# Kernel optimization log

Measured on AMD Instinct MI355X. Metric: run time of the kernel, lower is better.

The kernel has to match this reference:

```python
import jax, jax.numpy as jnp
import numpy as np

N_NODES = 50000


def gcn_conv(x, src, dst, W, b, n_nodes):
    """PyG-style GCNConv: x' = D^-1/2 (A + I) D^-1/2 (x W) + b.
    src/dst already include self-loops."""
    h = x @ W  # [N, C_out]
    # symmetric normalization from degree (with self-loops, unit edge weight)
    deg = jax.ops.segment_sum(jnp.ones_like(dst, dtype=h.dtype), dst,
                              num_segments=n_nodes)  # [N]
    dinv = jnp.where(deg > 0, jax.lax.rsqrt(deg), 0.0)
    norm = dinv[src] * dinv[dst]  # [E]
    msg = h[src] * norm[:, None]  # gather + scale, [E, C_out]
    out = jax.ops.segment_sum(msg, dst, num_segments=n_nodes)  # scatter-add
    return out + b


def setup_inputs() -> dict:
    key = jax.random.key(0)
    k1, k2, k3, k4, k5, k6 = jax.random.split(key, 6)
    in_c, hid_c, out_c = 128, 64, 64
    x = jax.random.normal(k1, (N_NODES, in_c), dtype=jnp.float32)
    edge_index = jax.random.randint(k2, (2, 800000), 0, N_NODES, dtype=jnp.int64)
    # Glorot-ish init for weights, zeros for bias (as PyG default)
    W1 = jax.random.normal(k3, (in_c, hid_c), dtype=jnp.float32) / np.sqrt(in_c)
    b1 = jnp.zeros((hid_c,), dtype=jnp.float32)
    W2 = jax.random.normal(k4, (hid_c, out_c), dtype=jnp.float32) / np.sqrt(hid_c)
    b2 = jnp.zeros((out_c,), dtype=jnp.float32)
    return {"x": x, "edge_index": edge_index, "W1": W1, "b1": b1,
            "W2": W2, "b2": b2}


def reference(x, edge_index, W1, b1, W2, b2):
    n = x.shape[0]
    loops = jnp.arange(n, dtype=edge_index.dtype)
    src = jnp.concatenate([edge_index[0], loops])  # add self-loops
    dst = jnp.concatenate([edge_index[1], loops])
    h = gcn_conv(x, src, dst, W1, b1, n)
    h = jax.nn.relu(h)
    return gcn_conv(h, src, dst, W2, b2, n)
```

## Files before the change

kernel.cpp:

```cpp
#include <hip/hip_runtime.h>
#include <hip/hip_fp16.h>


#define C_HID 64
#define NCHUNK 512
#define ES3 1280
#define ES4 768

static inline size_t alignup(size_t x) { return (x + 255) & ~(size_t)255; }

typedef __attribute__((address_space(3))) unsigned int lds_uint;
typedef __attribute__((address_space(1))) const unsigned int glob_uint;

__device__ __forceinline__ int blockScanIncl256(int v, int* wsum) {
    const int lane = threadIdx.x & 63, wav = threadIdx.x >> 6;
    int s = v;
#pragma unroll
    for (int off = 1; off < 64; off <<= 1) {
        int t = __shfl_up(s, off);
        if (lane >= off) s += t;
    }
    if (lane == 63) wsum[wav] = s;
    __syncthreads();
    if (wav == 0 && lane < 4) {
        int ws = wsum[lane];
#pragma unroll
        for (int off = 1; off < 4; off <<= 1) {
            int t = __shfl_up(ws, off);
            if (lane >= off) ws += t;
        }
        wsum[lane] = ws;
    }
    __syncthreads();
    return (wav ? wsum[wav - 1] : 0) + s;
}

template <int K>
__global__ __launch_bounds__(256) void gemm1_hist_kernel(
    const float* __restrict__ X, const float* __restrict__ W,
    const int* __restrict__ dst, __half* __restrict__ outh,
    int* __restrict__ S, int n, int E, int ePer, int nb) {
    constexpr int KP = K + 4;
    __shared__ float Xs[64 * KP];
    __shared__ float Ws[K * 64];
    __shared__ int h[1024];
    const int t = threadIdx.x;
    const int lane = t & 63;
    const int wav = t >> 6;

    if ((int)blockIdx.x < NCHUNK) {
        for (int i = t; i < nb; i += 256) h[i] = 0;
        __syncthreads();
        int beg = blockIdx.x * ePer, end = min(E, beg + ePer);
        for (int e = beg + t; e < end; e += 256)
            atomicAdd(&h[dst[e] >> 6], 1);
        __syncthreads();
        for (int b = t; b < nb; b += 256)
            S[(size_t)b * NCHUNK + blockIdx.x] = h[b];
        return;
    }

    const int row0 = ((int)blockIdx.x - NCHUNK) * 64;
    {
        const char* gb = (const char*)W;
        char* lb = (char*)Ws;
        for (int off = wav * 1024; off < K * 64 * 4; off += 4096)
            __builtin_amdgcn_global_load_lds((glob_uint*)(gb + off + lane * 16),
                                             (lds_uint*)(lb + off), 16, 0, 0);
    }
    if (row0 + 64 <= n) {
        const float4* g4 = (const float4*)(X + (size_t)row0 * K);
        for (int i = t; i < 64 * (K / 4); i += 256) {
            float4 v = g4[i];
            int r = i / (K / 4), k0 = (i % (K / 4)) * 4;
            *(float4*)&Xs[r * KP + k0] = v;
        }
    } else {
        for (int i = t; i < 64 * K; i += 256) {
            int r = i / K, k = i % K;
            Xs[r * KP + k] = (row0 + r < n) ? X[(size_t)(row0 + r) * K + k] : 0.0f;
        }
    }
    __syncthreads();

    const int tx = t & 15;
    const int ty = t >> 4;
    float acc[4][4] = {{0.f}};
#pragma unroll 2
    for (int k0 = 0; k0 < K; k0 += 4) {
        float4 a0 = *(const float4*)&Xs[(4 * ty + 0) * KP + k0];
        float4 a1 = *(const float4*)&Xs[(4 * ty + 1) * KP + k0];
        float4 a2 = *(const float4*)&Xs[(4 * ty + 2) * KP + k0];
        float4 a3 = *(const float4*)&Xs[(4 * ty + 3) * KP + k0];
        float4 b0 = *(const float4*)&Ws[(k0 + 0) * 64 + 4 * tx];
        float4 b1 = *(const float4*)&Ws[(k0 + 1) * 64 + 4 * tx];
        float4 b2 = *(const float4*)&Ws[(k0 + 2) * 64 + 4 * tx];
        float4 b3 = *(const float4*)&Ws[(k0 + 3) * 64 + 4 * tx];
        const float* ap[4] = {(const float*)&a0, (const float*)&a1,
                              (const float*)&a2, (const float*)&a3};
        const float* bp[4] = {(const float*)&b0, (const float*)&b1,
                              (const float*)&b2, (const float*)&b3};
#pragma unroll
        for (int r = 0; r < 4; ++r)
#pragma unroll
            for (int kk = 0; kk < 4; ++kk) {
                float av = ap[r][kk];
#pragma unroll
                for (int c = 0; c < 4; ++c)
                    acc[r][c] = fmaf(av, bp[kk][c], acc[r][c]);
            }
    }
#pragma unroll
    for (int r = 0; r < 4; ++r) {
        int row = row0 + 4 * ty + r;
        if (row < n) {
            __half2 p01 = __floats2half2_rn(acc[r][0], acc[r][1]);
            __half2 p23 = __floats2half2_rn(acc[r][2], acc[r][3]);
            float2 st;
            ((__half2*)&st)[0] = p01;
            ((__half2*)&st)[1] = p23;
            *(float2*)&outh[(size_t)row * 64 + 4 * tx] = st;
        }
    }
}

__global__ __launch_bounds__(256) void scan_rows_kernel(
    int* __restrict__ S, int* __restrict__ T) {
    __shared__ int wsum[4];
    const int b = blockIdx.x, t = threadIdx.x;
    int4 v = make_int4(0, 0, 0, 0);
    if (t < NCHUNK / 4) v = ((const int4*)(S + (size_t)b * NCHUNK))[t];
    int p1 = v.x + v.y, p2 = p1 + v.z, p3 = p2 + v.w;
    int incl = blockScanIncl256(p3, wsum);
    int excl = incl - p3;
    if (t < NCHUNK / 4) {
        int4 o;
        o.x = excl; o.y = excl + v.x; o.z = excl + p1; o.w = excl + p2;
        ((int4*)(S + (size_t)b * NCHUNK))[t] = o;
    }
    if (t == 0) T[b] = wsum[3];
}

__global__ __launch_bounds__(256) void scatter_kernel(
    const int* __restrict__ src, const int* __restrict__ dst, int E, int ePer,
    const int* __restrict__ S, const int* __restrict__ T,
    unsigned* __restrict__ ebuf, int nb) {
    __shared__ int tmp[1024];
    __shared__ int arr[1024];
    __shared__ int wsum[4];
    const int b = blockIdx.x, t = threadIdx.x;
    {
        int a0 = (4 * t + 0 < nb) ? T[4 * t + 0] : 0;
        int a1 = (4 * t + 1 < nb) ? T[4 * t + 1] : 0;
        int a2 = (4 * t + 2 < nb) ? T[4 * t + 2] : 0;
        int a3 = (4 * t + 3 < nb) ? T[4 * t + 3] : 0;
        int p1 = a0 + a1, p2 = p1 + a2, p3 = p2 + a3;
        int incl = blockScanIncl256(p3, wsum);
        int excl = incl - p3;
        tmp[4 * t + 0] = excl;
        tmp[4 * t + 1] = excl + a0;
        tmp[4 * t + 2] = excl + p1;
        tmp[4 * t + 3] = excl + p2;
    }
    __syncthreads();
    for (int i = t; i < nb; i += 256)
        arr[i] = S[(size_t)i * NCHUNK + b] + tmp[i];
    __syncthreads();
    int beg = b * ePer, end = min(E, beg + ePer);
    for (int e = beg + t; e < end; e += 256) {
        int d = dst[e];
        int s = src[e];
        int pos = atomicAdd(&arr[d >> 6], 1);
        ebuf[pos] = ((unsigned)s << 6) | (unsigned)(d & 63);
    }
}

__global__ __launch_bounds__(256) void build_kernel(
    const unsigned* __restrict__ ebuf, const int* __restrict__ T,
    int* __restrict__ row_ptr, float* __restrict__ dinv,
    int* __restrict__ esrc, __half* __restrict__ g1, int n, int nb) {
    __shared__ int tmp[1024];
    __shared__ int cnt[64];
    __shared__ int cur[64];
    __shared__ float dvs[64];
    __shared__ int wsum[4];
    const int b = blockIdx.x, t = threadIdx.x;
    {
        int a0 = (4 * t + 0 < nb) ? T[4 * t + 0] : 0;
        int a1 = (4 * t + 1 < nb) ? T[4 * t + 1] : 0;
        int a2 = (4 * t + 2 < nb) ? T[4 * t + 2] : 0;
        int a3 = (4 * t + 3 < nb) ? T[4 * t + 3] : 0;
        int p1 = a0 + a1, p2 = p1 + a2, p3 = p2 + a3;
        int incl = blockScanIncl256(p3, wsum);
        int excl = incl - p3;
        tmp[4 * t + 0] = excl + a0;
        tmp[4 * t + 1] = excl + p1;
        tmp[4 * t + 2] = excl + p2;
        tmp[4 * t + 3] = excl + p3;
    }
    if (t < 64) cnt[t] = 0;
    __syncthreads();
    const int ebeg = b ? tmp[b - 1] : 0;
    const int eend = tmp[b];

    for (int e = ebeg + t; e < eend; e += 256)
        atomicAdd(&cnt[ebuf[e] & 63], 1);
    __syncthreads();
    if (t < 64) {
        int deg = cnt[t];
        int s = deg;
#pragma unroll
        for (int off = 1; off < 64; off <<= 1) {
            int x = __shfl_up(s, off);
            if (t >= off) s += x;
        }
        cur[t] = ebeg + s - deg;
        float dv = rsqrtf(1.0f + (float)deg);
        dvs[t] = dv;
        int v = (b << 6) + t;
        if (v < n) {
            row_ptr[v + 1] = ebeg + s;
            dinv[v] = dv;
            if (v == 0) row_ptr[0] = 0;
        }
    }
    __syncthreads();
    for (int e = ebeg + t; e < eend; e += 256) {
        unsigned p = ebuf[e];
        int pos = atomicAdd(&cur[p & 63], 1);
        esrc[pos] = (int)(p >> 6);
    }
    {
        const int row = t >> 2, q = t & 3;
        const int v = (b << 6) + row;
        if (v < n) {
            float dv = dvs[row];
            float4* gp = (float4*)(g1 + (size_t)v * 64 + q * 16);
            float4 r0 = gp[0], r1 = gp[1];
            __half2* h0 = (__half2*)&r0;
            __half2* h1 = (__half2*)&r1;
#pragma unroll
            for (int i2 = 0; i2 < 4; ++i2) {
                float2 f0 = __half22float2(h0[i2]);
                float2 f1 = __half22float2(h1[i2]);
                h0[i2] = __floats2half2_rn(f0.x * dv, f0.y * dv);
                h1[i2] = __floats2half2_rn(f1.x * dv, f1.y * dv);
            }
            gp[0] = r0;
            gp[1] = r1;
        }
    }
}

template <bool LDSE>
__device__ __forceinline__ void agg1_body(
    const float4* __restrict__ hs4, const int* es, const int* __restrict__ esg,
    int beg0, int beg, int end, int c, float acc[16]) {
    int j = beg;
    for (; j + 4 <= end; j += 4) {
        int s0, s1, s2, s3;
        if (LDSE) {
            s0 = es[j]; s1 = es[j + 1]; s2 = es[j + 2]; s3 = es[j + 3];
        } else {
            s0 = esg[beg0 + j]; s1 = esg[beg0 + j + 1];
            s2 = esg[beg0 + j + 2]; s3 = esg[beg0 + j + 3];
        }
        size_t rb0 = (size_t)s0 * 8 + 2 * c, rb1 = (size_t)s1 * 8 + 2 * c;
        size_t rb2 = (size_t)s2 * 8 + 2 * c, rb3 = (size_t)s3 * 8 + 2 * c;
        float4 a0 = hs4[rb0], a1 = hs4[rb0 + 1];
        float4 b0 = hs4[rb1], b1v = hs4[rb1 + 1];
        float4 c0 = hs4[rb2], c1 = hs4[rb2 + 1];
        float4 e0 = hs4[rb3], e1 = hs4[rb3 + 1];
        const __half2 *pa0 = (const __half2*)&a0, *pa1 = (const __half2*)&a1;
        const __half2 *pb0 = (const __half2*)&b0, *pb1 = (const __half2*)&b1v;
        const __half2 *pc0 = (const __half2*)&c0, *pc1 = (const __half2*)&c1;
        const __half2 *pe0 = (const __half2*)&e0, *pe1 = (const __half2*)&e1;
#pragma unroll
        for (int q = 0; q < 4; ++q) {
            float2 f;
            f = __half22float2(pa0[q]); acc[2 * q] += f.x; acc[2 * q + 1] += f.y;
            f = __half22float2(pa1[q]); acc[8 + 2 * q] += f.x; acc[9 + 2 * q] += f.y;
            f = __half22float2(pb0[q]); acc[2 * q] += f.x; acc[2 * q + 1] += f.y;
            f = __half22float2(pb1[q]); acc[8 + 2 * q] += f.x; acc[9 + 2 * q] += f.y;
            f = __half22float2(pc0[q]); acc[2 * q] += f.x; acc[2 * q + 1] += f.y;
            f = __half22float2(pc1[q]); acc[8 + 2 * q] += f.x; acc[9 + 2 * q] += f.y;
            f = __half22float2(pe0[q]); acc[2 * q] += f.x; acc[2 * q + 1] += f.y;
            f = __half22float2(pe1[q]); acc[8 + 2 * q] += f.x; acc[9 + 2 * q] += f.y;
        }
    }
    for (; j < end; ++j) {
        int s0 = LDSE ? es[j] : esg[beg0 + j];
        size_t rb0 = (size_t)s0 * 8 + 2 * c;
        float4 a0 = hs4[rb0], a1 = hs4[rb0 + 1];
        const __half2 *pa0 = (const __half2*)&a0, *pa1 = (const __half2*)&a1;
#pragma unroll
        for (int q = 0; q < 4; ++q) {
            float2 f;
            f = __half22float2(pa0[q]); acc[2 * q] += f.x; acc[2 * q + 1] += f.y;
            f = __half22float2(pa1[q]); acc[8 + 2 * q] += f.x; acc[9 + 2 * q] += f.y;
        }
    }
}

__global__ __launch_bounds__(256) void agg1_gemm2_kernel(
    const __half* __restrict__ g1, const int* __restrict__ row_ptr,
    const int* __restrict__ esrc, const float* __restrict__ dinv,
    const float* __restrict__ b1, const float* __restrict__ W2,
    __half* __restrict__ g2, int n) {
    __shared__ float Bt[64][68];
    __shared__ float Ws2[64 * 64];
    __shared__ int es[ES3];
    const int t = threadIdx.x, lane = t & 63, wav = t >> 6;
    const int row0 = blockIdx.x * 64;

    const int beg0 = row_ptr[row0];
    const int end0 = row_ptr[min(row0 + 64, n)];
    const int tot = end0 - beg0;
    const bool uselds = (tot <= ES3);
    if (uselds)
        for (int i = t; i < tot; i += 256) es[i] = esrc[beg0 + i];
    __syncthreads();

    {
        const char* gb = (const char*)W2;
        char* lb = (char*)Ws2;
        for (int off = wav * 1024; off < 64 * 64 * 4; off += 4096)
            __builtin_amdgcn_global_load_lds((glob_uint*)(gb + off + lane * 16),
                                             (lds_uint*)(lb + off), 16, 0, 0);
    }

    const int g = t >> 2;
    const int c = t & 3;
    const int v = row0 + g;
    const float4* __restrict__ hs4 = (const float4*)g1;

    if (v < n) {
        float acc[16];
        {
            size_t rb = (size_t)v * 8 + 2 * c;
            float4 r0 = hs4[rb], r1 = hs4[rb + 1];
            const __half2* h0 = (const __half2*)&r0;
            const __half2* h1 = (const __half2*)&r1;
#pragma unroll
            for (int q = 0; q < 4; ++q) {
                float2 f0 = __half22float2(h0[q]);
                float2 f1 = __half22float2(h1[q]);
                acc[2 * q] = f0.x;     acc[2 * q + 1] = f0.y;
                acc[8 + 2 * q] = f1.x; acc[9 + 2 * q] = f1.y;
            }
        }
        const int beg = row_ptr[v] - beg0;
        const int end = row_ptr[v + 1] - beg0;
        if (uselds) agg1_body<true>(hs4, es, esrc, beg0, beg, end, c, acc);
        else        agg1_body<false>(hs4, es, esrc, beg0, beg, end, c, acc);
        const float dv0 = dinv[v];
        const float* bb = b1 + c * 16;
#pragma unroll
        for (int u = 0; u < 4; ++u) {
            float4 w;
            w.x = fmaxf(fmaf(acc[4 * u + 0], dv0, bb[4 * u + 0]), 0.f);
            w.y = fmaxf(fmaf(acc[4 * u + 1], dv0, bb[4 * u + 1]), 0.f);
            w.z = fmaxf(fmaf(acc[4 * u + 2], dv0, bb[4 * u + 2]), 0.f);
            w.w = fmaxf(fmaf(acc[4 * u + 3], dv0, bb[4 * u + 3]), 0.f);
            *(float4*)&Bt[g][c * 16 + 4 * u] = w;
        }
    } else {
#pragma unroll
        for (int u = 0; u < 4; ++u)
            *(float4*)&Bt[g][c * 16 + 4 * u] = make_float4(0.f, 0.f, 0.f, 0.f);
    }
    __syncthreads();

    const int tx = t & 15;
    const int ty = t >> 4;
    float a2[4][4] = {{0.f}};
#pragma unroll 2
    for (int k0 = 0; k0 < 64; k0 += 4) {
        float4 x0 = *(const float4*)&Bt[4 * ty + 0][k0];
        float4 x1 = *(const float4*)&Bt[4 * ty + 1][k0];
        float4 x2 = *(const float4*)&Bt[4 * ty + 2][k0];
        float4 x3 = *(const float4*)&Bt[4 * ty + 3][k0];
        float4 w0 = *(const float4*)&Ws2[(k0 + 0) * 64 + 4 * tx];
        float4 w1 = *(const float4*)&Ws2[(k0 + 1) * 64 + 4 * tx];
        float4 w2 = *(const float4*)&Ws2[(k0 + 2) * 64 + 4 * tx];
        float4 w3 = *(const float4*)&Ws2[(k0 + 3) * 64 + 4 * tx];
        const float* xp[4] = {(const float*)&x0, (const float*)&x1,
                              (const float*)&x2, (const float*)&x3};
        const float* wp[4] = {(const float*)&w0, (const float*)&w1,
                              (const float*)&w2, (const float*)&w3};
#pragma unroll
        for (int r = 0; r < 4; ++r)
#pragma unroll
            for (int kk = 0; kk < 4; ++kk) {
                float av = xp[r][kk];
#pragma unroll
                for (int cc = 0; cc < 4; ++cc)
                    a2[r][cc] = fmaf(av, wp[kk][cc], a2[r][cc]);
            }
    }
#pragma unroll
    for (int r = 0; r < 4; ++r) {
        int row = row0 + 4 * ty + r;
        if (row < n) {
            float dv = dinv[row];
            __half2 p01 = __floats2half2_rn(a2[r][0] * dv, a2[r][1] * dv);
            __half2 p23 = __floats2half2_rn(a2[r][2] * dv, a2[r][3] * dv);
            float2 st;
            ((__half2*)&st)[0] = p01;
            ((__half2*)&st)[1] = p23;
            *(float2*)&g2[(size_t)row * 64 + 4 * tx] = st;
        }
    }
}

template <bool LDSE>
__device__ __forceinline__ void agg2_body(
    const float4* __restrict__ hs4, const int* es, const int* __restrict__ esg,
    int beg0, int beg, int end, int c8, float acc[8]) {
    int j = beg;
    for (; j + 4 <= end; j += 4) {
        int s0, s1, s2, s3;
        if (LDSE) {
            s0 = es[j]; s1 = es[j + 1]; s2 = es[j + 2]; s3 = es[j + 3];
        } else {
            s0 = esg[beg0 + j]; s1 = esg[beg0 + j + 1];
            s2 = esg[beg0 + j + 2]; s3 = esg[beg0 + j + 3];
        }
        float4 r0 = hs4[(size_t)s0 * 8 + c8];
        float4 r1 = hs4[(size_t)s1 * 8 + c8];
        float4 r2 = hs4[(size_t)s2 * 8 + c8];
        float4 r3 = hs4[(size_t)s3 * 8 + c8];
        const __half2* h0 = (const __half2*)&r0;
        const __half2* h1 = (const __half2*)&r1;
        const __half2* h2 = (const __half2*)&r2;
        const __half2* h3 = (const __half2*)&r3;
#pragma unroll
        for (int q = 0; q < 4; ++q) {
            float2 f0 = __half22float2(h0[q]);
            float2 f1 = __half22float2(h1[q]);
            float2 f2 = __half22float2(h2[q]);
            float2 f3 = __half22float2(h3[q]);
            acc[2 * q]     += (f0.x + f1.x) + (f2.x + f3.x);
            acc[2 * q + 1] += (f0.y + f1.y) + (f2.y + f3.y);
        }
    }
    for (; j < end; ++j) {
        int s0 = LDSE ? es[j] : esg[beg0 + j];
        float4 r0 = hs4[(size_t)s0 * 8 + c8];
        const __half2* h0 = (const __half2*)&r0;
#pragma unroll
        for (int q = 0; q < 4; ++q) {
            float2 f0 = __half22float2(h0[q]);
            acc[2 * q] += f0.x;
            acc[2 * q + 1] += f0.y;
        }
    }
}

__global__ __launch_bounds__(256) void aggregate2_kernel(
    const __half* __restrict__ hs,
    const int* __restrict__ row_ptr,
    const int* __restrict__ esrc,
    const float* __restrict__ dinv,
    const float* __restrict__ bias,
    float* __restrict__ out, int n) {
    __shared__ int es[ES4];
    const int t = threadIdx.x;
    const int row0 = blockIdx.x * 32;
    const int beg0 = row_ptr[row0];
    const int end0 = row_ptr[min(row0 + 32, n)];
    const int tot = end0 - beg0;
    const bool uselds = (tot <= ES4);
    if (uselds)
        for (int i = t; i < tot; i += 256) es[i] = esrc[beg0 + i];
    __syncthreads();

    const int v = row0 + (t >> 3);
    if (v >= n) return;
    const int c8 = t & 7;
    const float4* __restrict__ hs4 = (const float4*)hs;

    float acc[8];
    {
        float4 raw = hs4[(size_t)v * 8 + c8];
        const __half2* hp = (const __half2*)&raw;
#pragma unroll
        for (int q = 0; q < 4; ++q) {
            float2 f = __half22float2(hp[q]);
            acc[2 * q] = f.x; acc[2 * q + 1] = f.y;
        }
    }

    const int beg = row_ptr[v] - beg0;
    const int end = row_ptr[v + 1] - beg0;
    if (uselds) agg2_body<true>(hs4, es, esrc, beg0, beg, end, c8, acc);
    else        agg2_body<false>(hs4, es, esrc, beg0, beg, end, c8, acc);

    float dv = dinv[v];
    float4 b0 = *(const float4*)(bias + c8 * 8);
    float4 b1v = *(const float4*)(bias + c8 * 8 + 4);
    float4 o0, o1;
    o0.x = fmaf(acc[0], dv, b0.x); o0.y = fmaf(acc[1], dv, b0.y);
    o0.z = fmaf(acc[2], dv, b0.z); o0.w = fmaf(acc[3], dv, b0.w);
    o1.x = fmaf(acc[4], dv, b1v.x); o1.y = fmaf(acc[5], dv, b1v.y);
    o1.z = fmaf(acc[6], dv, b1v.z); o1.w = fmaf(acc[7], dv, b1v.w);
    float4* op = (float4*)(out + (size_t)v * 64 + c8 * 8);
    op[0] = o0;
    op[1] = o1;
}

extern "C" void kernel_launch(void* const* d_in, const int* in_sizes, int n_in,
                              void* d_out, int out_size, void* d_ws, size_t ws_size,
                              hipStream_t stream) {
    const float* x  = (const float*)d_in[0];
    const int*   ei = (const int*)d_in[1];
    const float* W1 = (const float*)d_in[2];
    const float* b1 = (const float*)d_in[3];
    const float* W2 = (const float*)d_in[4];
    const float* b2 = (const float*)d_in[5];
    float* out = (float*)d_out;

    const int C_IN = 128;
    const int n = in_sizes[0] / C_IN;
    const int E = in_sizes[1] / 2;
    const int* src = ei;
    const int* dst = ei + E;

    const int nb = (n + 63) >> 6;
    const int ngb = (n + 63) / 64;
    const int ePer = (E + NCHUNK - 1) / NCHUNK;

    char* w = (char*)d_ws;
    float*    dinv    = (float*)w;    w += alignup((size_t)n * sizeof(float));
    __half*   g1      = (__half*)w;   w += alignup((size_t)n * C_HID * sizeof(__half));
    __half*   g2      = (__half*)w;   w += alignup((size_t)n * C_HID * sizeof(__half));
    int*      row_ptr = (int*)w;      w += alignup((size_t)(n + 1) * sizeof(int));
    int*      S       = (int*)w;      w += alignup((size_t)nb * NCHUNK * sizeof(int));
    int*      T       = (int*)w;      w += alignup((size_t)(nb + 1) * sizeof(int));
    unsigned* ebuf    = (unsigned*)w; w += alignup((size_t)E * sizeof(unsigned));
    int*      esrc    = (int*)w;

    gemm1_hist_kernel<128><<<NCHUNK + ngb, 256, 0, stream>>>(
        x, W1, dst, g1, S, n, E, ePer, nb);

    scan_rows_kernel<<<nb, 256, 0, stream>>>(S, T);
    scatter_kernel<<<NCHUNK, 256, 0, stream>>>(src, dst, E, ePer, S, T, ebuf, nb);
    build_kernel<<<nb, 256, 0, stream>>>(ebuf, T, row_ptr, dinv, esrc, g1, n, nb);

    agg1_gemm2_kernel<<<ngb, 256, 0, stream>>>(
        g1, row_ptr, esrc, dinv, b1, W2, g2, n);

    aggregate2_kernel<<<(n + 31) / 32, 256, 0, stream>>>(
        g2, row_ptr, esrc, dinv, b2, out, n);
}
```

Measured before the change: 163.9 us.

## Fuse scan, scatter, build and both aggregations into one persistent kernel with grid barriers

Replaces five separate launches (row scan, scatter, CSR build, agg1+gemm2, aggregate2) with one persistent 512-block kernel. The phases are separated by a software grid barrier built on an atomic counter, which the histogram kernel resets. The aim is to remove launch gaps and tail effects between the small dependent stages. Chunk count rises to 784 and layer-2 aggregation now uses 64-row tiles with four threads per row. The barrier depends on all 512 blocks being co-resident, which is risky, and blocks now loop serially over tiles.

```diff
diff --git a/kernel.cpp b/kernel.cpp
--- a/kernel.cpp
+++ b/kernel.cpp
@@ -3,14 +3,26 @@
 
 
 #define C_HID 64
-#define NCHUNK 512
+#define NCHUNK 784
+#define GMEGA 512
 #define ES3 1280
-#define ES4 768
 
 static inline size_t alignup(size_t x) { return (x + 255) & ~(size_t)255; }
 
 typedef __attribute__((address_space(3))) unsigned int lds_uint;
 typedef __attribute__((address_space(1))) const unsigned int glob_uint;
+
+__device__ __forceinline__ void gsync(unsigned* bar, unsigned target) {
+    __syncthreads();
+    if (threadIdx.x == 0) {
+        __threadfence();
+        atomicAdd(bar, 1u);
+        while (atomicAdd(bar, 0u) < target)
+            __builtin_amdgcn_s_sleep(8);
+        __threadfence();
+    }
+    __syncthreads();
+}
 
 __device__ __forceinline__ int blockScanIncl256(int v, int* wsum) {
     const int lane = threadIdx.x & 63, wav = threadIdx.x >> 6;
@@ -39,7 +51,8 @@
 __global__ __launch_bounds__(256) void gemm1_hist_kernel(
     const float* __restrict__ X, const float* __restrict__ W,
     const int* __restrict__ dst, __half* __restrict__ outh,
-    int* __restrict__ S, int n, int E, int ePer, int nb) {
+    int* __restrict__ S, unsigned* __restrict__ bar,
+    int n, int E, int ePer, int nb) {
     constexpr int KP = K + 4;
     __shared__ float Xs[64 * KP];
     __shared__ float Ws[K * 64];
@@ -49,6 +62,7 @@
     const int wav = t >> 6;
 
     if ((int)blockIdx.x < NCHUNK) {
+        if (blockIdx.x == 0 && t == 0) *bar = 0;
         for (int i = t; i < nb; i += 256) h[i] = 0;
         __syncthreads();
         int beg = blockIdx.x * ePer, end = min(E, beg + ePer);
@@ -124,134 +138,6 @@
     }
 }
 
-__global__ __launch_bounds__(256) void scan_rows_kernel(
-    int* __restrict__ S, int* __restrict__ T) {
-    __shared__ int wsum[4];
-    const int b = blockIdx.x, t = threadIdx.x;
-    int4 v = make_int4(0, 0, 0, 0);
-    if (t < NCHUNK / 4) v = ((const int4*)(S + (size_t)b * NCHUNK))[t];
-    int p1 = v.x + v.y, p2 = p1 + v.z, p3 = p2 + v.w;
-    int incl = blockScanIncl256(p3, wsum);
-    int excl = incl - p3;
-    if (t < NCHUNK / 4) {
-        int4 o;
-        o.x = excl; o.y = excl + v.x; o.z = excl + p1; o.w = excl + p2;
-        ((int4*)(S + (size_t)b * NCHUNK))[t] = o;
-    }
-    if (t == 0) T[b] = wsum[3];
-}
-
-__global__ __launch_bounds__(256) void scatter_kernel(
-    const int* __restrict__ src, const int* __restrict__ dst, int E, int ePer,
-    const int* __restrict__ S, const int* __restrict__ T,
-    unsigned* __restrict__ ebuf, int nb) {
-    __shared__ int tmp[1024];
-    __shared__ int arr[1024];
-    __shared__ int wsum[4];
-    const int b = blockIdx.x, t = threadIdx.x;
-    {
-        int a0 = (4 * t + 0 < nb) ? T[4 * t + 0] : 0;
-        int a1 = (4 * t + 1 < nb) ? T[4 * t + 1] : 0;
-        int a2 = (4 * t + 2 < nb) ? T[4 * t + 2] : 0;
-        int a3 = (4 * t + 3 < nb) ? T[4 * t + 3] : 0;
-        int p1 = a0 + a1, p2 = p1 + a2, p3 = p2 + a3;
-        int incl = blockScanIncl256(p3, wsum);
-        int excl = incl - p3;
-        tmp[4 * t + 0] = excl;
-        tmp[4 * t + 1] = excl + a0;
-        tmp[4 * t + 2] = excl + p1;
-        tmp[4 * t + 3] = excl + p2;
-    }
-    __syncthreads();
-    for (int i = t; i < nb; i += 256)
-        arr[i] = S[(size_t)i * NCHUNK + b] + tmp[i];
-    __syncthreads();
-    int beg = b * ePer, end = min(E, beg + ePer);
-    for (int e = beg + t; e < end; e += 256) {
-        int d = dst[e];
-        int s = src[e];
-        int pos = atomicAdd(&arr[d >> 6], 1);
-        ebuf[pos] = ((unsigned)s << 6) | (unsigned)(d & 63);
-    }
-}
-
-__global__ __launch_bounds__(256) void build_kernel(
-    const unsigned* __restrict__ ebuf, const int* __restrict__ T,
-    int* __restrict__ row_ptr, float* __restrict__ dinv,
-    int* __restrict__ esrc, __half* __restrict__ g1, int n, int nb) {
-    __shared__ int tmp[1024];
-    __shared__ int cnt[64];
-    __shared__ int cur[64];
-    __shared__ float dvs[64];
-    __shared__ int wsum[4];
-    const int b = blockIdx.x, t = threadIdx.x;
-    {
-        int a0 = (4 * t + 0 < nb) ? T[4 * t + 0] : 0;
-        int a1 = (4 * t + 1 < nb) ? T[4 * t + 1] : 0;
-        int a2 = (4 * t + 2 < nb) ? T[4 * t + 2] : 0;
-        int a3 = (4 * t + 3 < nb) ? T[4 * t + 3] : 0;
-        int p1 = a0 + a1, p2 = p1 + a2, p3 = p2 + a3;
-        int incl = blockScanIncl256(p3, wsum);
-        int excl = incl - p3;
-        tmp[4 * t + 0] = excl + a0;
-        tmp[4 * t + 1] = excl + p1;
-        tmp[4 * t + 2] = excl + p2;
-        tmp[4 * t + 3] = excl + p3;
-    }
-    if (t < 64) cnt[t] = 0;
-    __syncthreads();
-    const int ebeg = b ? tmp[b - 1] : 0;
-    const int eend = tmp[b];
-
-    for (int e = ebeg + t; e < eend; e += 256)
-        atomicAdd(&cnt[ebuf[e] & 63], 1);
-    __syncthreads();
-    if (t < 64) {
-        int deg = cnt[t];
-        int s = deg;
-#pragma unroll
-        for (int off = 1; off < 64; off <<= 1) {
-            int x = __shfl_up(s, off);
-            if (t >= off) s += x;
-        }
-        cur[t] = ebeg + s - deg;
-        float dv = rsqrtf(1.0f + (float)deg);
-        dvs[t] = dv;
-        int v = (b << 6) + t;
-        if (v < n) {
-            row_ptr[v + 1] = ebeg + s;
-            dinv[v] = dv;
-            if (v == 0) row_ptr[0] = 0;
-        }
-    }
-    __syncthreads();
-    for (int e = ebeg + t; e < eend; e += 256) {
-        unsigned p = ebuf[e];
-        int pos = atomicAdd(&cur[p & 63], 1);
-        esrc[pos] = (int)(p >> 6);
-    }
-    {
-        const int row = t >> 2, q = t & 3;
-        const int v = (b << 6) + row;
-        if (v < n) {
-            float dv = dvs[row];
-            float4* gp = (float4*)(g1 + (size_t)v * 64 + q * 16);
-            float4 r0 = gp[0], r1 = gp[1];
-            __half2* h0 = (__half2*)&r0;
-            __half2* h1 = (__half2*)&r1;
-#pragma unroll
-            for (int i2 = 0; i2 < 4; ++i2) {
-                float2 f0 = __half22float2(h0[i2]);
-                float2 f1 = __half22float2(h1[i2]);
-                h0[i2] = __floats2half2_rn(f0.x * dv, f0.y * dv);
-                h1[i2] = __floats2half2_rn(f1.x * dv, f1.y * dv);
-            }
-            gp[0] = r0;
-            gp[1] = r1;
-        }
-    }
-}
-
 template <bool LDSE>
 __device__ __forceinline__ void agg1_body(
     const float4* __restrict__ hs4, const int* es, const int* __restrict__ esg,
@@ -302,211 +188,288 @@
     }
 }
 
-__global__ __launch_bounds__(256) void agg1_gemm2_kernel(
-    const __half* __restrict__ g1, const int* __restrict__ row_ptr,
-    const int* __restrict__ esrc, const float* __restrict__ dinv,
-    const float* __restrict__ b1, const float* __restrict__ W2,
-    __half* __restrict__ g2, int n) {
-    __shared__ float Bt[64][68];
-    __shared__ float Ws2[64 * 64];
-    __shared__ int es[ES3];
+__global__ __launch_bounds__(256, 4) void mega_kernel(
+    const int* __restrict__ src, const int* __restrict__ dst, int E, int ePer,
+    int* __restrict__ S, int* __restrict__ T, unsigned* __restrict__ ebuf,
+    int* __restrict__ row_ptr, float* __restrict__ dinv, int* __restrict__ esrc,
+    __half* __restrict__ g1, const float* __restrict__ b1,
+    const float* __restrict__ W2, __half* __restrict__ g2,
+    const float* __restrict__ b2, float* __restrict__ out,
+    unsigned* __restrict__ bar, int n, int nb) {
+    __shared__ union SM {
+        struct { int tmp[1024]; int arr[1024]; } c;
+        struct { int tmp[1024]; int cnt[64]; int cur[64]; float dvs[64]; } d;
+        struct { float Bt[64][68]; float Ws2[64 * 64]; int es[ES3]; } e;
+        struct { int es[ES3]; } f;
+    } sm;
+    __shared__ int wsum[4];
     const int t = threadIdx.x, lane = t & 63, wav = t >> 6;
-    const int row0 = blockIdx.x * 64;
-
-    const int beg0 = row_ptr[row0];
-    const int end0 = row_ptr[min(row0 + 64, n)];
-    const int tot = end0 - beg0;
-    const bool uselds = (tot <= ES3);
-    if (uselds)
-        for (int i = t; i < tot; i += 256) es[i] = esrc[beg0 + i];
-    __syncthreads();
+    const int ngb = nb;
+    const int G = gridDim.x;
+
+    for (int b = blockIdx.x; b < nb; b += G) {
+        int4 v = make_int4(0, 0, 0, 0);
+        if (t < NCHUNK / 4) v = ((const int4*)(S + (size_t)b * NCHUNK))[t];
+        int p1 = v.x + v.y, p2 = p1 + v.z, p3 = p2 + v.w;
+        int incl = blockScanIncl256(p3, wsum);
+        int excl = incl - p3;
+        if (t < NCHUNK / 4) {
+            int4 o;
+            o.x = excl; o.y = excl + v.x; o.z = excl + p1; o.w = excl + p2;
+            ((int4*)(S + (size_t)b * NCHUNK))[t] = o;
+        }
+        if (t == 0) T[b] = wsum[3];
+        __syncthreads();
+    }
+    gsync(bar, 1u * G);
 
     {
         const char* gb = (const char*)W2;
-        char* lb = (char*)Ws2;
+        char* lb = (char*)sm.e.Ws2;
         for (int off = wav * 1024; off < 64 * 64 * 4; off += 4096)
             __builtin_amdgcn_global_load_lds((glob_uint*)(gb + off + lane * 16),
                                              (lds_uint*)(lb + off), 16, 0, 0);
     }
 
+    {
+        int a0 = (4 * t + 0 < nb) ? T[4 * t + 0] : 0;
+        int a1 = (4 * t + 1 < nb) ? T[4 * t + 1] : 0;
+        int a2 = (4 * t + 2 < nb) ? T[4 * t + 2] : 0;
+        int a3 = (4 * t + 3 < nb) ? T[4 * t + 3] : 0;
+        int p1 = a0 + a1, p2 = p1 + a2, p3 = p2 + a3;
+        int incl = blockScanIncl256(p3, wsum);
+        int excl = incl - p3;
+        sm.c.tmp[4 * t + 0] = excl;
+        sm.c.tmp[4 * t + 1] = excl + a0;
+        sm.c.tmp[4 * t + 2] = excl + p1;
+        sm.c.tmp[4 * t + 3] = excl + p2;
+    }
+    __syncthreads();
+    for (int b = blockIdx.x; b < NCHUNK; b += G) {
+        for (int i = t; i < nb; i += 256)
+            sm.c.arr[i] = S[(size_t)i * NCHUNK + b] + sm.c.tmp[i];
+        __syncthreads();
+        int beg = b * ePer, end = min(E, beg + ePer);
+        for (int e = beg + t; e < end; e += 256) {
+            int d = dst[e];
+            int s = src[e];
+            int pos = atomicAdd(&sm.c.arr[d >> 6], 1);
+            ebuf[pos] = ((unsigned)s << 6) | (unsigned)(d & 63);
+        }
+        __syncthreads();
+    }
+    gsync(bar, 2u * G);
+
+    {
+        int a0 = (4 * t + 0 < nb) ? T[4 * t + 0] : 0;
+        int a1 = (4 * t + 1 < nb) ? T[4 * t + 1] : 0;
+        int a2 = (4 * t + 2 < nb) ? T[4 * t + 2] : 0;
+        int a3 = (4 * t + 3 < nb) ? T[4 * t + 3] : 0;
+        int p1 = a0 + a1, p2 = p1 + a2, p3 = p2 + a3;
+        int incl = blockScanIncl256(p3, wsum);
+        int excl = incl - p3;
+        sm.d.tmp[4 * t + 0] = excl + a0;
+        sm.d.tmp[4 * t + 1] = excl + p1;
+        sm.d.tmp[4 * t + 2] = excl + p2;
+        sm.d.tmp[4 * t + 3] = excl + p3;
+    }
+    __syncthreads();
+    for (int b = blockIdx.x; b < nb; b += G) {
+        if (t < 64) sm.d.cnt[t] = 0;
+        __syncthreads();
+        const int ebeg = b ? sm.d.tmp[b - 1] : 0;
+        const int eend = sm.d.tmp[b];
+        for (int e = ebeg + t; e < eend; e += 256)
+            atomicAdd(&sm.d.cnt[ebuf[e] & 63], 1);
+        __syncthreads();
+        if (t < 64) {
+            int deg = sm.d.cnt[t];
+            int s = deg;
+#pragma unroll
+            for (int off = 1; off < 64; off <<= 1) {
+                int x = __shfl_up(s, off);
+                if (t >= off) s += x;
+            }
+            sm.d.cur[t] = ebeg + s - deg;
+            float dv = rsqrtf(1.0f + (float)deg);
+            sm.d.dvs[t] = dv;
+            int v = (b << 6) + t;
+            if (v < n) {
+                row_ptr[v + 1] = ebeg + s;
+                dinv[v] = dv;
+                if (v == 0) row_ptr[0] = 0;
+            }
+        }
+        __syncthreads();
+        for (int e = ebeg + t; e < eend; e += 256) {
+            unsigned p = ebuf[e];
+            int pos = atomicAdd(&sm.d.cur[p & 63], 1);
+            esrc[pos] = (int)(p >> 6);
+        }
+        {
+            const int row = t >> 2, q = t & 3;
+            const int v = (b << 6) + row;
+            if (v < n) {
+                float dv = sm.d.dvs[row];
+                float4* gp = (float4*)(g1 + (size_t)v * 64 + q * 16);
+                float4 r0 = gp[0], r1 = gp[1];
+                __half2* h0 = (__half2*)&r0;
+                __half2* h1 = (__half2*)&r1;
+#pragma unroll
+                for (int i2 = 0; i2 < 4; ++i2) {
+                    float2 f0 = __half22float2(h0[i2]);
+                    float2 f1 = __half22float2(h1[i2]);
+                    h0[i2] = __floats2half2_rn(f0.x * dv, f0.y * dv);
+                    h1[i2] = __floats2half2_rn(f1.x * dv, f1.y * dv);
+                }
+                gp[0] = r0;
+                gp[1] = r1;
+            }
+        }
+        __syncthreads();
+    }
+    gsync(bar, 3u * G);
+
     const int g = t >> 2;
-    const int c = t & 3;
-    const int v = row0 + g;
-    const float4* __restrict__ hs4 = (const float4*)g1;
-
-    if (v < n) {
-        float acc[16];
-        {
-            size_t rb = (size_t)v * 8 + 2 * c;
-            float4 r0 = hs4[rb], r1 = hs4[rb + 1];
-            const __half2* h0 = (const __half2*)&r0;
-            const __half2* h1 = (const __half2*)&r1;
-#pragma unroll
-            for (int q = 0; q < 4; ++q) {
-                float2 f0 = __half22float2(h0[q]);
-                float2 f1 = __half22float2(h1[q]);
-                acc[2 * q] = f0.x;     acc[2 * q + 1] = f0.y;
-                acc[8 + 2 * q] = f1.x; acc[9 + 2 * q] = f1.y;
-            }
-        }
-        const int beg = row_ptr[v] - beg0;
-        const int end = row_ptr[v + 1] - beg0;
-        if (uselds) agg1_body<true>(hs4, es, esrc, beg0, beg, end, c, acc);
-        else        agg1_body<false>(hs4, es, esrc, beg0, beg, end, c, acc);
-        const float dv0 = dinv[v];
-        const float* bb = b1 + c * 16;
-#pragma unroll
-        for (int u = 0; u < 4; ++u) {
-            float4 w;
-            w.x = fmaxf(fmaf(acc[4 * u + 0], dv0, bb[4 * u + 0]), 0.f);
-            w.y = fmaxf(fmaf(acc[4 * u + 1], dv0, bb[4 * u + 1]), 0.f);
-            w.z = fmaxf(fmaf(acc[4 * u + 2], dv0, bb[4 * u + 2]), 0.f);
-            w.w = fmaxf(fmaf(acc[4 * u + 3], dv0, bb[4 * u + 3]), 0.f);
-            *(float4*)&Bt[g][c * 16 + 4 * u] = w;
-        }
-    } else {
-#pragma unroll
-        for (int u = 0; u < 4; ++u)
-            *(float4*)&Bt[g][c * 16 + 4 * u] = make_float4(0.f, 0.f, 0.f, 0.f);
-    }
-    __syncthreads();
-
-    const int tx = t & 15;
-    const int ty = t >> 4;
-    float a2[4][4] = {{0.f}};
+    const int c4 = t & 3;
+    const float4* __restrict__ h1s4 = (const float4*)g1;
+    for (int bb = blockIdx.x; bb < ngb; bb += G) {
+        const int row0 = bb * 64;
+        const int beg0 = row_ptr[row0];
+        const int end0 = row_ptr[min(row0 + 64, n)];
+        const int tot = end0 - beg0;
+        const bool uselds = (tot <= ES3);
+        if (uselds)
+            for (int i = t; i < tot; i += 256) sm.e.es[i] = esrc[beg0 + i];
+        __syncthreads();
+
+        const int v = row0 + g;
+        if (v < n) {
+            float acc[16];
+            {
+                size_t rb = (size_t)v * 8 + 2 * c4;
+                float4 r0 = h1s4[rb], r1 = h1s4[rb + 1];
+                const __half2* h0 = (const __half2*)&r0;
+                const __half2* h1 = (const __half2*)&r1;
+#pragma unroll
+                for (int q = 0; q < 4; ++q) {
+                    float2 f0 = __half22float2(h0[q]);
+                    float2 f1 = __half22float2(h1[q]);
+                    acc[2 * q] = f0.x;     acc[2 * q + 1] = f0.y;
+                    acc[8 + 2 * q] = f1.x; acc[9 + 2 * q] = f1.y;
+                }
+            }
+            const int beg = row_ptr[v] - beg0;
+            const int end = row_ptr[v + 1] - beg0;
+            if (uselds) agg1_body<true>(h1s4, sm.e.es, esrc, beg0, beg, end, c4, acc);
+            else        agg1_body<false>(h1s4, sm.e.es, esrc, beg0, beg, end, c4, acc);
+            const float dv0 = dinv[v];
+            const float* bb1 = b1 + c4 * 16;
+#pragma unroll
+            for (int u = 0; u < 4; ++u) {
+                float4 w;
+                w.x = fmaxf(fmaf(acc[4 * u + 0], dv0, bb1[4 * u + 0]), 0.f);
+                w.y = fmaxf(fmaf(acc[4 * u + 1], dv0, bb1[4 * u + 1]), 0.f);
+                w.z = fmaxf(fmaf(acc[4 * u + 2], dv0, bb1[4 * u + 2]), 0.f);
+                w.w = fmaxf(fmaf(acc[4 * u + 3], dv0, bb1[4 * u + 3]), 0.f);
+                *(float4*)&sm.e.Bt[g][c4 * 16 + 4 * u] = w;
+            }
+        } else {
+#pragma unroll
+            for (int u = 0; u < 4; ++u)
+                *(float4*)&sm.e.Bt[g][c4 * 16 + 4 * u] = make_float4(0.f, 0.f, 0.f, 0.f);
+        }
+        __syncthreads();
+
+        const int tx = t & 15;
+        const int ty = t >> 4;
+        float a2[4][4] = {{0.f}};
 #pragma unroll 2
-    for (int k0 = 0; k0 < 64; k0 += 4) {
-        float4 x0 = *(const float4*)&Bt[4 * ty + 0][k0];
-        float4 x1 = *(const float4*)&Bt[4 * ty + 1][k0];
-        float4 x2 = *(const float4*)&Bt[4 * ty + 2][k0];
-        float4 x3 = *(const float4*)&Bt[4 * ty + 3][k0];
-        float4 w0 = *(const float4*)&Ws2[(k0 + 0) * 64 + 4 * tx];
-        float4 w1 = *(const float4*)&Ws2[(k0 + 1) * 64 + 4 * tx];
-        float4 w2 = *(const float4*)&Ws2[(k0 + 2) * 64 + 4 * tx];
-        float4 w3 = *(const float4*)&Ws2[(k0 + 3) * 64 + 4 * tx];
-        const float* xp[4] = {(const float*)&x0, (const float*)&x1,
-                              (const float*)&x2, (const float*)&x3};
-        const float* wp[4] = {(const float*)&w0, (const float*)&w1,
-                              (const float*)&w2, (const float*)&w3};
-#pragma unroll
-        for (int r = 0; r < 4; ++r)
-#pragma unroll
-            for (int kk = 0; kk < 4; ++kk) {
-                float av = xp[r][kk];
-#pragma unroll
-                for (int cc = 0; cc < 4; ++cc)
-                    a2[r][cc] = fmaf(av, wp[kk][cc], a2[r][cc]);
-            }
-    }
-#pragma unroll
-    for (int r = 0; r < 4; ++r) {
-        int row = row0 + 4 * ty + r;
-        if (row < n) {
-            float dv = dinv[row];
-            __half2 p01 = __floats2half2_rn(a2[r][0] * dv, a2[r][1] * dv);
-            __half2 p23 = __floats2half2_rn(a2[r][2] * dv, a2[r][3] * dv);
-            float2 st;
-            ((__half2*)&st)[0] = p01;
-            ((__half2*)&st)[1] = p23;
-            *(float2*)&g2[(size_t)row * 64 + 4 * tx] = st;
-        }
-    }
-}
-
-template <bool LDSE>
-__device__ __forceinline__ void agg2_body(
-    const float4* __restrict__ hs4, const int* es, const int* __restrict__ esg,
-    int beg0, int beg, int end, int c8, float acc[8]) {
-    int j = beg;
-    for (; j + 4 <= end; j += 4) {
-        int s0, s1, s2, s3;
-        if (LDSE) {
-            s0 = es[j]; s1 = es[j + 1]; s2 = es[j + 2]; s3 = es[j + 3];
-        } else {
-            s0 = esg[beg0 + j]; s1 = esg[beg0 + j + 1];
-            s2 = esg[beg0 + j + 2]; s3 = esg[beg0 + j + 3];
-        }
-        float4 r0 = hs4[(size_t)s0 * 8 + c8];
-        float4 r1 = hs4[(size_t)s1 * 8 + c8];
-        float4 r2 = hs4[(size_t)s2 * 8 + c8];
-        float4 r3 = hs4[(size_t)s3 * 8 + c8];
-        const __half2* h0 = (const __half2*)&r0;
-        const __half2* h1 = (const __half2*)&r1;
-        const __half2* h2 = (const __half2*)&r2;
-        const __half2* h3 = (const __half2*)&r3;
-#pragma unroll
-        for (int q = 0; q < 4; ++q) {
-            float2 f0 = __half22float2(h0[q]);
-            float2 f1 = __half22float2(h1[q]);
-            float2 f2 = __half22float2(h2[q]);
-            float2 f3 = __half22float2(h3[q]);
-            acc[2 * q]     += (f0.x + f1.x) + (f2.x + f3.x);
-            acc[2 * q + 1] += (f0.y + f1.y) + (f2.y + f3.y);
-        }
-    }
-    for (; j < end; ++j) {
-        int s0 = LDSE ? es[j] : esg[beg0 + j];
-        float4 r0 = hs4[(size_t)s0 * 8 + c8];
-        const __half2* h0 = (const __half2*)&r0;
-#pragma unroll
-        for (int q = 0; q < 4; ++q) {
-            float2 f0 = __half22float2(h0[q]);
-            acc[2 * q] += f0.x;
-            acc[2 * q + 1] += f0.y;
-        }
-    }
-}
-
-__global__ __launch_bounds__(256) void aggregate2_kernel(
-    const __half* __restrict__ hs,
-    const int* __restrict__ row_ptr,
-    const int* __restrict__ esrc,
-    const float* __restrict__ dinv,
-    const float* __restrict__ bias,
-    float* __restrict__ out, int n) {
-    __shared__ int es[ES4];
-    const int t = threadIdx.x;
-    const int row0 = blockIdx.x * 32;
-    const int beg0 = row_ptr[row0];
-    const int end0 = row_ptr[min(row0 + 32, n)];
-    const int tot = end0 - beg0;
-    const bool uselds = (tot <= ES4);
-    if (uselds)
-        for (int i = t; i < tot; i += 256) es[i] = esrc[beg0 + i];
-    __syncthreads();
-
-    const int v = row0 + (t >> 3);
-    if (v >= n) return;
-    const int c8 = t & 7;
-    const float4* __restrict__ hs4 = (const float4*)hs;
-
-    float acc[8];
-    {
-        float4 raw = hs4[(size_t)v * 8 + c8];
-        const __half2* hp = (const __half2*)&raw;
-#pragma unroll
-        for (int q = 0; q < 4; ++q) {
-            float2 f = __half22float2(hp[q]);
-            acc[2 * q] = f.x; acc[2 * q + 1] = f.y;
-        }
-    }
-
-    const int beg = row_ptr[v] - beg0;
-    const int end = row_ptr[v + 1] - beg0;
-    if (uselds) agg2_body<true>(hs4, es, esrc, beg0, beg, end, c8, acc);
-    else        agg2_body<false>(hs4, es, esrc, beg0, beg, end, c8, acc);
-
-    float dv = dinv[v];
-    float4 b0 = *(const float4*)(bias + c8 * 8);
-    float4 b1v = *(const float4*)(bias + c8 * 8 + 4);
-    float4 o0, o1;
-    o0.x = fmaf(acc[0], dv, b0.x); o0.y = fmaf(acc[1], dv, b0.y);
-    o0.z = fmaf(acc[2], dv, b0.z); o0.w = fmaf(acc[3], dv, b0.w);
-    o1.x = fmaf(acc[4], dv, b1v.x); o1.y = fmaf(acc[5], dv, b1v.y);
-    o1.z = fmaf(acc[6], dv, b1v.z); o1.w = fmaf(acc[7], dv, b1v.w);
-    float4* op = (float4*)(out + (size_t)v * 64 + c8 * 8);
-    op[0] = o0;
-    op[1] = o1;
+        for (int k0 = 0; k0 < 64; k0 += 4) {
+            float4 x0 = *(const float4*)&sm.e.Bt[4 * ty + 0][k0];
+            float4 x1 = *(const float4*)&sm.e.Bt[4 * ty + 1][k0];
+            float4 x2 = *(const float4*)&sm.e.Bt[4 * ty + 2][k0];
+            float4 x3 = *(const float4*)&sm.e.Bt[4 * ty + 3][k0];
+            float4 w0 = *(const float4*)&sm.e.Ws2[(k0 + 0) * 64 + 4 * tx];
+            float4 w1 = *(const float4*)&sm.e.Ws2[(k0 + 1) * 64 + 4 * tx];
+            float4 w2 = *(const float4*)&sm.e.Ws2[(k0 + 2) * 64 + 4 * tx];
+            float4 w3 = *(const float4*)&sm.e.Ws2[(k0 + 3) * 64 + 4 * tx];
+            const float* xp[4] = {(const float*)&x0, (const float*)&x1,
+                                  (const float*)&x2, (const float*)&x3};
+            const float* wp[4] = {(const float*)&w0, (const float*)&w1,
+                                  (const float*)&w2, (const float*)&w3};
+#pragma unroll
+            for (int r = 0; r < 4; ++r)
+#pragma unroll
+                for (int kk = 0; kk < 4; ++kk) {
+                    float av = xp[r][kk];
+#pragma unroll
+                    for (int cc = 0; cc < 4; ++cc)
+                        a2[r][cc] = fmaf(av, wp[kk][cc], a2[r][cc]);
+                }
+        }
+#pragma unroll
+        for (int r = 0; r < 4; ++r) {
+            int row = row0 + 4 * ty + r;
+            if (row < n) {
+                float dv = dinv[row];
+                __half2 p01 = __floats2half2_rn(a2[r][0] * dv, a2[r][1] * dv);
+                __half2 p23 = __floats2half2_rn(a2[r][2] * dv, a2[r][3] * dv);
+                float2 st;
+                ((__half2*)&st)[0] = p01;
+                ((__half2*)&st)[1] = p23;
+                *(float2*)&g2[(size_t)row * 64 + 4 * tx] = st;
+            }
+        }
+        __syncthreads();
+    }
+    gsync(bar, 4u * G);
+
+    const float4* __restrict__ h2s4 = (const float4*)g2;
+    for (int bb = blockIdx.x; bb < ngb; bb += G) {
+        const int row0 = bb * 64;
+        const int beg0 = row_ptr[row0];
+        const int end0 = row_ptr[min(row0 + 64, n)];
+        const int tot = end0 - beg0;
+        const bool uselds = (tot <= ES3);
+        if (uselds)
+            for (int i = t; i < tot; i += 256) sm.f.es[i] = esrc[beg0 + i];
+        __syncthreads();
+
+        const int v = row0 + g;
+        if (v < n) {
+            float acc[16];
+            {
+                size_t rb = (size_t)v * 8 + 2 * c4;
+                float4 r0 = h2s4[rb], r1 = h2s4[rb + 1];
+                const __half2* h0 = (const __half2*)&r0;
+                const __half2* h1 = (const __half2*)&r1;
+#pragma unroll
+                for (int q = 0; q < 4; ++q) {
+                    float2 f0 = __half22float2(h0[q]);
+                    float2 f1 = __half22float2(h1[q]);
+                    acc[2 * q] = f0.x;     acc[2 * q + 1] = f0.y;
+                    acc[8 + 2 * q] = f1.x; acc[9 + 2 * q] = f1.y;
+                }
+            }
+            const int beg = row_ptr[v] - beg0;
+            const int end = row_ptr[v + 1] - beg0;
+            if (uselds) agg1_body<true>(h2s4, sm.f.es, esrc, beg0, beg, end, c4, acc);
+            else        agg1_body<false>(h2s4, sm.f.es, esrc, beg0, beg, end, c4, acc);
+            const float dv = dinv[v];
+#pragma unroll
+            for (int u = 0; u < 4; ++u) {
+                float4 bv = *(const float4*)(b2 + c4 * 16 + 4 * u);
+                float4 o;
+                o.x = fmaf(acc[4 * u + 0], dv, bv.x);
+                o.y = fmaf(acc[4 * u + 1], dv, bv.y);
+                o.z = fmaf(acc[4 * u + 2], dv, bv.z);
+                o.w = fmaf(acc[4 * u + 3], dv, bv.w);
+                *(float4*)(out + (size_t)v * 64 + c4 * 16 + 4 * u) = o;
+            }
+        }
+        __syncthreads();
+    }
 }
 
 extern "C" void kernel_launch(void* const* d_in, const int* in_sizes, int n_in,
@@ -538,18 +501,13 @@
     int*      S       = (int*)w;      w += alignup((size_t)nb * NCHUNK * sizeof(int));
     int*      T       = (int*)w;      w += alignup((size_t)(nb + 1) * sizeof(int));
     unsigned* ebuf    = (unsigned*)w; w += alignup((size_t)E * sizeof(unsigned));
-    int*      esrc    = (int*)w;
+    int*      esrc    = (int*)w;      w += alignup((size_t)E * sizeof(int));
+    unsigned* bar     = (unsigned*)w;
 
     gemm1_hist_kernel<128><<<NCHUNK + ngb, 256, 0, stream>>>(
-        x, W1, dst, g1, S, n, E, ePer, nb);
-
-    scan_rows_kernel<<<nb, 256, 0, stream>>>(S, T);
-    scatter_kernel<<<NCHUNK, 256, 0, stream>>>(src, dst, E, ePer, S, T, ebuf, nb);
-    build_kernel<<<nb, 256, 0, stream>>>(ebuf, T, row_ptr, dinv, esrc, g1, n, nb);
-
-    agg1_gemm2_kernel<<<ngb, 256, 0, stream>>>(
-        g1, row_ptr, esrc, dinv, b1, W2, g2, n);
-
-    aggregate2_kernel<<<(n + 31) / 32, 256, 0, stream>>>(
-        g2, row_ptr, esrc, dinv, b2, out, n);
+        x, W1, dst, g1, S, bar, n, E, ePer, nb);
+
+    mega_kernel<<<GMEGA, 256, 0, stream>>>(
+        src, dst, E, ePer, S, T, ebuf, row_ptr, dinv, esrc,
+        g1, b1, W2, g2, b2, out, bar, n, nb);
 }
```

Measured after the change: 418.4 us. 155% more time.
